# Kernel tuning notes

Measured on AMD Instinct MI355X. Metric: run time of the kernel, lower is better.

The kernel has to match this reference:

```python
import jax, jax.numpy as jnp
import numpy as np
import math

EPS = 1e-6
N_NODES = 25000
N_EDGES = 400000
F = 8            # multivector channels
NB = 8           # blades of Cl(3,0)
NORM_FACTOR = 1.0
SUBSPACES = np.array([1, 3, 3, 1])
REP = np.repeat(np.arange(4), SUBSPACES)   # grade index per blade: [0,1,1,1,2,2,2,3]
GRADES = np.array([0, 1, 1, 1, 2, 2, 2, 3])

def _build_cayley():
    # shortlex blade order for dim 3: 1, e1, e2, e3, e12, e13, e23, e123
    bitmaps = [0, 1, 2, 4, 3, 5, 6, 7]
    b2i = {b: i for i, b in enumerate(bitmaps)}
    def sign(a, b):
        a >>= 1
        s = 0
        while a:
            s += bin(a & b).count('1')
            a >>= 1
        return 1.0 if s % 2 == 0 else -1.0  # euclidean metric (1,1,1)
    C = np.zeros((NB, NB, NB), np.float32)
    for i, bi in enumerate(bitmaps):
        for j, bj in enumerate(bitmaps):
            C[i, b2i[bi ^ bj], j] = sign(bi, bj)   # cayley[left, out, right]
    return C

CAYLEY_NP = _build_cayley()

def _paths():
    p = np.zeros((4, 4, 4), bool)
    for a in range(4):
        for b in range(4):
            for c in range(4):
                blk = CAYLEY_NP[GRADES == a][:, GRADES == b][:, :, GRADES == c]
                p[a, b, c] = np.any(blk != 0)
    return np.nonzero(p)

PI, PJ, PK = _paths()
N_PATHS = len(PI)  # 20 for Cl(3,0)
CAYLEY = jnp.asarray(CAYLEY_NP)

def grade_qs(x):
    # per-grade quadratic form (euclidean: sum of squares), x: [..., 8] -> [..., 4]
    sq = x * x
    return jnp.concatenate([sq[..., 0:1],
                            sq[..., 1:4].sum(-1, keepdims=True),
                            sq[..., 4:7].sum(-1, keepdims=True),
                            sq[..., 7:8]], axis=-1)

def mv_linear(x, w, b=None):
    # w: [out, in, 4] grade-wise weights, repeat-interleaved over blades
    out = jnp.einsum('bmi,nmi->bni', x, w[:, :, REP])
    if b is not None:
        out = out.at[:, :, 0].add(b[0, :, 0])   # bias embedded in scalar blade
    return out

def mv_silu(x, a, b):
    q = grade_qs(x)
    inv = jnp.concatenate([x[..., :1], q[..., 1:]], axis=-1)  # scalar + mag2 per grade
    gate = jax.nn.sigmoid(a * inv + b)[..., REP]
    return gate * x

def sgp(x, w_right, w_geo, w_left, b_left, a_norm):
    # SteerableGeometricProductLayer with NormalizationLayer on the right input
    xr = mv_linear(x, w_right)
    norms = jnp.sqrt(grade_qs(xr))                       # [B,F,4]
    norms = jax.nn.sigmoid(a_norm) * (norms - 1.0) + 1.0
    xr = xr / (norms[..., REP] + EPS)
    W4 = jnp.zeros((F, 4, 4, 4), x.dtype).at[:, PI, PJ, PK].set(w_geo)
    W8 = W4[:, REP][:, :, REP][:, :, :, REP] * CAYLEY    # [F,8,8,8]
    geo = jnp.einsum('bni,nijk,bnk->bnj', x, W8, xr)
    return (mv_linear(x, w_left, b_left) + geo) / math.sqrt(2.0)

def mv_layernorm(x, a):
    n = jnp.sqrt((x * x).sum(-1, keepdims=True)).mean(axis=1, keepdims=True) + EPS
    return a[..., None] * x / n

def block(x, lin_w, lin_b, silu_a, silu_b, gp_wr, gp_w, gp_wl, gp_bl, gp_an, ln_a):
    # CEMLP block: MVLinear -> MVSiLU -> SteerableGeometricProduct -> MVLayerNorm
    x = mv_linear(x, lin_w, lin_b)
    x = mv_silu(x, silu_a, silu_b)
    x = sgp(x, gp_wr, gp_w, gp_wl, gp_bl, gp_an)
    return mv_layernorm(x, ln_a)

def setup_inputs() -> dict:
    key = jax.random.key(0)
    ks = jax.random.split(key, 12)
    h = jax.random.normal(ks[0], (N_NODES, F, NB), jnp.float32)
    edge_index = jax.random.randint(ks[1], (2, N_EDGES), 0, N_NODES)
    def linw(k, out_f, in_f):
        return jax.random.normal(k, (out_f, in_f, 4), jnp.float32) / math.sqrt(in_f)
    inp = dict(h=h, edge_index=edge_index)
    for pref, kk in (('e', 2), ('n', 7)):
        inp[pref + '_lin_w'] = linw(ks[kk], F, 2 * F)
        inp[pref + '_lin_b'] = jnp.zeros((1, F, 1), jnp.float32)
        inp[pref + '_silu_a'] = jnp.ones((1, F, 4), jnp.float32)
        inp[pref + '_silu_b'] = jnp.zeros((1, F, 4), jnp.float32)
        inp[pref + '_gp_wr'] = linw(ks[kk + 1], F, F)
        inp[pref + '_gp_w'] = jax.random.normal(ks[kk + 2], (F, N_PATHS), jnp.float32) / 2.0
        inp[pref + '_gp_wl'] = linw(ks[kk + 3], F, F)
        inp[pref + '_gp_bl'] = jnp.zeros((1, F, 1), jnp.float32)
        inp[pref + '_gp_an'] = jnp.zeros((F, 4), jnp.float32)
        inp[pref + '_ln_a'] = jnp.ones((1, F), jnp.float32)
    return inp

def reference(h, edge_index,
              e_lin_w, e_lin_b, e_silu_a, e_silu_b, e_gp_wr, e_gp_w, e_gp_wl, e_gp_bl, e_gp_an, e_ln_a,
              n_lin_w, n_lin_b, n_silu_a, n_silu_b, n_gp_wr, n_gp_w, n_gp_wl, n_gp_bl, n_gp_an, n_ln_a):
    row, col = edge_index[0], edge_index[1]
    # edge model: gather endpoint features, Clifford MLP block
    m = jnp.concatenate([h[row], h[col]], axis=1)          # [E, 2F, 8]
    m = block(m, e_lin_w, e_lin_b, e_silu_a, e_silu_b,
              e_gp_wr, e_gp_w, e_gp_wl, e_gp_bl, e_gp_an, e_ln_a)
    # unsorted_segment_sum on flattened multivectors, 'sum' aggregation
    agg = jax.ops.segment_sum(m.reshape(N_EDGES, -1), row, num_segments=N_NODES) / NORM_FACTOR
    agg = agg.reshape(N_NODES, F, NB)
    # node update: residual Clifford MLP block on [h, agg]
    upd = jnp.concatenate([h, agg], axis=1)                # [N, 2F, 8]
    upd = block(upd, n_lin_w, n_lin_b, n_silu_a, n_silu_b,
                n_gp_wr, n_gp_w, n_gp_wl, n_gp_bl, n_gp_an, n_ln_a)
    return h + upd
```

## Files before the change

kernel.cpp:

```cpp
#include <hip/hip_runtime.h>

#define NNODES 25000
#define NEDGES 400000
#define EPB 32
#define XSTR2 68
#define EPSF 1e-6f
#define RSQRT2 0.7071067811865476f

typedef _Float16 half8 __attribute__((ext_vector_type(8)));

static constexpr int GJ[64] = {
 0,1,2,3,4,5,6,7,
 1,0,4,5,2,3,7,6,
 2,4,0,6,1,7,3,5,
 3,5,6,0,7,1,2,4,
 4,2,1,7,0,6,5,3,
 5,3,7,1,6,0,4,2,
 6,7,3,2,5,4,0,1,
 7,6,5,4,3,2,1,0};
static constexpr int GS[64] = {
 1, 1, 1, 1, 1, 1, 1, 1,
 1, 1, 1, 1, 1, 1, 1, 1,
 1,-1, 1, 1,-1,-1, 1,-1,
 1,-1,-1, 1, 1,-1,-1, 1,
 1,-1, 1, 1,-1,-1, 1,-1,
 1,-1,-1, 1, 1,-1,-1, 1,
 1, 1,-1, 1,-1, 1,-1,-1,
 1, 1,-1, 1,-1, 1,-1,-1};
static constexpr int GP[64] = {
  0, 1, 1, 1, 2, 2, 2, 3,
  5, 4, 7, 7, 6, 6, 9, 8,
  5, 7, 4, 7, 6, 9, 6, 8,
  5, 7, 7, 4, 9, 6, 6, 8,
 13,11,11,15,10,14,14,12,
 13,11,15,11,14,10,14,12,
 13,15,11,11,14,14,10,12,
 19,18,18,18,17,17,17,16};

struct WP {
  const float *wlin, *blin, *asi, *bsi, *wr, *wg, *wl, *bl, *an, *aln;
};

__device__ __forceinline__ float sigm(float x) {
  return __builtin_amdgcn_rcpf(1.f + __expf(-x));
}
__device__ __forceinline__ float frcp(float x) { return __builtin_amdgcn_rcpf(x); }
__device__ __forceinline__ float fsqrt(float x) { return __builtin_amdgcn_sqrtf(x); }

__device__ __forceinline__ void wave_fence() {
  asm volatile("s_waitcnt lgkmcnt(0)" ::: "memory");
  __builtin_amdgcn_sched_barrier(0);
}

#define C_WR   0
#define C_WL   (C_WR + 288)
#define C_WG   (C_WL + 288)
#define C_BLIN (C_WG + 160)
#define C_ASI  (C_BLIN + 8)
#define C_BSI  (C_ASI + 32)
#define C_BL   (C_BSI + 32)
#define C_SA   (C_BL + 8)
#define C_SCC  (C_SA + 32)
#define C_ALN  (C_SCC + 32)
#define C_TOT  (C_ALN + 8)
#define C_WLIN C_TOT
#define CN_TOT (C_WLIN + 8*68)

__device__ __forceinline__ void stage_common(int tid, float* Ws, const WP& wp) {
  int t = tid;
  if (t < 256) Ws[C_WR + (t >> 5) * 36 + (t & 31)] = wp.wr[t];
  if (t < 256) Ws[C_WL + (t >> 5) * 36 + (t & 31)] = wp.wl[t];
  if (t < 160) Ws[C_WG + t] = wp.wg[t];
  if (t < 8)   Ws[C_BLIN + t] = wp.blin[t];
  if (t < 32)  Ws[C_ASI + t] = wp.asi[t];
  if (t < 32)  Ws[C_BSI + t] = wp.bsi[t];
  if (t < 8)   Ws[C_BL + t]  = wp.bl[t];
  if (t < 32)  {
    const float sv = sigm(wp.an[t]);
    Ws[C_SA + t]  = sv;
    Ws[C_SCC + t] = 1.f + EPSF - sv;
  }
  if (t < 8)   Ws[C_ALN + t] = wp.aln[t];
}

__device__ __forceinline__ void clifford_tail(float* __restrict__ X,
                                              const float* __restrict__ Ws,
                                              int n, const float* y, float* z)
{
  const float q1 = y[1]*y[1] + y[2]*y[2] + y[3]*y[3];
  const float q2 = y[4]*y[4] + y[5]*y[5] + y[6]*y[6];
  const float q3 = y[7]*y[7];
  const float g0 = sigm(Ws[C_ASI + n*4 + 0] * y[0] + Ws[C_BSI + n*4 + 0]);
  const float g1 = sigm(Ws[C_ASI + n*4 + 1] * q1  + Ws[C_BSI + n*4 + 1]);
  const float g2 = sigm(Ws[C_ASI + n*4 + 2] * q2  + Ws[C_BSI + n*4 + 2]);
  const float g3 = sigm(Ws[C_ASI + n*4 + 3] * q3  + Ws[C_BSI + n*4 + 3]);
  float s[8] = { g0*y[0], g1*y[1], g1*y[2], g1*y[3],
                 g2*y[4], g2*y[5], g2*y[6], g3*y[7] };
  *(float4*)&X[n*8]     = make_float4(s[0], s[1], s[2], s[3]);
  *(float4*)&X[n*8 + 4] = make_float4(s[4], s[5], s[6], s[7]);
  wave_fence();

  float xr[8], zl[8];
  #pragma unroll
  for (int i = 0; i < 8; ++i) { xr[i] = 0.f; zl[i] = 0.f; }
  #pragma unroll
  for (int m = 0; m < 8; ++m) {
    const float4 wr4 = *(const float4*)&Ws[C_WR + n * 36 + m * 4];
    const float4 wl4 = *(const float4*)&Ws[C_WL + n * 36 + m * 4];
    const float4 xa = *(const float4*)&X[m * 8];
    const float4 xb = *(const float4*)&X[m * 8 + 4];
    xr[0]=fmaf(xa.x,wr4.x,xr[0]); xr[1]=fmaf(xa.y,wr4.y,xr[1]); xr[2]=fmaf(xa.z,wr4.y,xr[2]); xr[3]=fmaf(xa.w,wr4.y,xr[3]);
    xr[4]=fmaf(xb.x,wr4.z,xr[4]); xr[5]=fmaf(xb.y,wr4.z,xr[5]); xr[6]=fmaf(xb.z,wr4.z,xr[6]); xr[7]=fmaf(xb.w,wr4.w,xr[7]);
    zl[0]=fmaf(xa.x,wl4.x,zl[0]); zl[1]=fmaf(xa.y,wl4.y,zl[1]); zl[2]=fmaf(xa.z,wl4.y,zl[2]); zl[3]=fmaf(xa.w,wl4.y,zl[3]);
    zl[4]=fmaf(xb.x,wl4.z,zl[4]); zl[5]=fmaf(xb.y,wl4.z,zl[5]); zl[6]=fmaf(xb.z,wl4.z,zl[6]); zl[7]=fmaf(xb.w,wl4.w,zl[7]);
  }
  zl[0] += Ws[C_BL + n];

  {
    const float t0 = fabsf(xr[0]);
    const float t1 = fsqrt(xr[1]*xr[1] + xr[2]*xr[2] + xr[3]*xr[3]);
    const float t2 = fsqrt(xr[4]*xr[4] + xr[5]*xr[5] + xr[6]*xr[6]);
    const float t3 = fabsf(xr[7]);
    const float d0 = frcp(fmaf(Ws[C_SA + n*4 + 0], t0, Ws[C_SCC + n*4 + 0]));
    const float d1 = frcp(fmaf(Ws[C_SA + n*4 + 1], t1, Ws[C_SCC + n*4 + 1]));
    const float d2 = frcp(fmaf(Ws[C_SA + n*4 + 2], t2, Ws[C_SCC + n*4 + 2]));
    const float d3 = frcp(fmaf(Ws[C_SA + n*4 + 3], t3, Ws[C_SCC + n*4 + 3]));
    xr[0] *= d0; xr[1] *= d1; xr[2] *= d1; xr[3] *= d1;
    xr[4] *= d2; xr[5] *= d2; xr[6] *= d2; xr[7] *= d3;
  }

  float geo[8];
  #pragma unroll
  for (int i = 0; i < 8; ++i) geo[i] = 0.f;
  {
    const int wgb = C_WG + n * 20;
    #pragma unroll
    for (int i = 0; i < 8; ++i) {
      #pragma unroll
      for (int k = 0; k < 8; ++k) {
        const float t = s[i] * xr[k];
        const float w = Ws[wgb + GP[i * 8 + k]];
        geo[GJ[i * 8 + k]] = fmaf(GS[i * 8 + k] > 0 ? w : -w, t, geo[GJ[i * 8 + k]]);
      }
    }
  }

  #pragma unroll
  for (int i = 0; i < 8; ++i) z[i] = (zl[i] + geo[i]) * RSQRT2;

  float sq = 0.f;
  #pragma unroll
  for (int i = 0; i < 8; ++i) sq = fmaf(z[i], z[i], sq);
  float nr = fsqrt(sq);
  nr += __shfl_xor(nr, 1);
  nr += __shfl_xor(nr, 2);
  nr += __shfl_xor(nr, 4);
  const float scale = Ws[C_ALN + n] * frcp(nr * 0.125f + EPSF);
  #pragma unroll
  for (int i = 0; i < 8; ++i) z[i] *= scale;
}

__global__ __launch_bounds__(1024)
void csr_scan_fast(const int* __restrict__ deg, int* __restrict__ ptr,
                   int* __restrict__ fill)
{
  __shared__ int wsum[16];
  const int t = threadIdx.x;
  const int base = t * 32;
  int d[32];
  int s = 0;
  #pragma unroll
  for (int i = 0; i < 8; ++i) {
    int idx = base + i * 4;
    int4 v = make_int4(0, 0, 0, 0);
    if (idx + 3 < NNODES) v = *(const int4*)(deg + idx);
    else {
      if (idx + 0 < NNODES) v.x = deg[idx + 0];
      if (idx + 1 < NNODES) v.y = deg[idx + 1];
      if (idx + 2 < NNODES) v.z = deg[idx + 2];
    }
    d[i*4+0] = v.x; d[i*4+1] = v.y; d[i*4+2] = v.z; d[i*4+3] = v.w;
    s += v.x + v.y + v.z + v.w;
  }
  const int lane = t & 63;
  int incl = s;
  #pragma unroll
  for (int off = 1; off < 64; off <<= 1) {
    int u = __shfl_up(incl, off);
    if (lane >= off) incl += u;
  }
  const int wv = t >> 6;
  if (lane == 63) wsum[wv] = incl;
  __syncthreads();
  if (t < 16) {
    int v = wsum[t];
    int inc = v;
    #pragma unroll
    for (int off = 1; off < 16; off <<= 1) {
      int u = __shfl_up(inc, off);
      if (t >= off) inc += u;
    }
    wsum[t] = inc - v;
  }
  __syncthreads();
  int run = wsum[wv] + (incl - s);
  #pragma unroll
  for (int i = 0; i < 8; ++i) {
    int idx = base + i * 4;
    int4 pv;
    pv.x = run; run += d[i*4+0];
    pv.y = run; run += d[i*4+1];
    pv.z = run; run += d[i*4+2];
    pv.w = run; run += d[i*4+3];
    if (idx + 3 < NNODES) {
      *(int4*)(ptr + idx)  = pv;
      *(int4*)(fill + idx) = pv;
    } else {
      if (idx + 0 < NNODES) { ptr[idx+0] = pv.x; fill[idx+0] = pv.x; }
      if (idx + 1 < NNODES) { ptr[idx+1] = pv.y; fill[idx+1] = pv.y; }
      if (idx + 2 < NNODES) { ptr[idx+2] = pv.z; fill[idx+2] = pv.z; }
    }
  }
  if (t == 1023) ptr[NNODES] = NEDGES;
}

#define PRE_BLOCKS ((NNODES + EPB - 1) / EPB)
#define CNT_BLOCKS ((NEDGES + 255) / 256)

__global__ __launch_bounds__(256)
void pre_count(const float* __restrict__ h,
               const float* __restrict__ wle,
               const float* __restrict__ ble,
               float* __restrict__ ue, float* __restrict__ ve,
               const int* __restrict__ eidx, int* __restrict__ deg)
{
  __shared__ __align__(16) float We[8 * 68];
  __shared__ __align__(16) float Xs[EPB * XSTR2];
  const int tid = threadIdx.x;

  if (blockIdx.x >= PRE_BLOCKS) {
    int e = (blockIdx.x - PRE_BLOCKS) * 256 + tid;
    if (e < NEDGES) atomicAdd(&deg[eidx[e]], 1);
    return;
  }

  for (int t = tid; t < 512; t += 256) We[(t >> 6) * 68 + (t & 63)] = wle[t];
  const int el = tid >> 3, n = tid & 7;
  const int item = blockIdx.x * EPB + el;
  float* X = &Xs[el * XSTR2];
  const bool act = item < NNODES;
  if (act) {
    const float4* ph = (const float4*)(h + (size_t)item * 64 + n * 8);
    *(float4*)&X[n * 8]     = ph[0];
    *(float4*)&X[n * 8 + 4] = ph[1];
  }
  __syncthreads();
  if (!act) return;
  float ua[8], va[8];
  #pragma unroll
  for (int i = 0; i < 8; ++i) { ua[i] = 0.f; va[i] = 0.f; }
  #pragma unroll
  for (int m = 0; m < 8; ++m) {
    const float4 xa = *(const float4*)&X[m * 8];
    const float4 xb = *(const float4*)&X[m * 8 + 4];
    const float4 wa = *(const float4*)&We[n * 68 + m * 4];
    const float4 wb = *(const float4*)&We[n * 68 + (m + 8) * 4];
    ua[0]=fmaf(xa.x,wa.x,ua[0]); ua[1]=fmaf(xa.y,wa.y,ua[1]); ua[2]=fmaf(xa.z,wa.y,ua[2]); ua[3]=fmaf(xa.w,wa.y,ua[3]);
    ua[4]=fmaf(xb.x,wa.z,ua[4]); ua[5]=fmaf(xb.y,wa.z,ua[5]); ua[6]=fmaf(xb.z,wa.z,ua[6]); ua[7]=fmaf(xb.w,wa.w,ua[7]);
    va[0]=fmaf(xa.x,wb.x,va[0]); va[1]=fmaf(xa.y,wb.y,va[1]); va[2]=fmaf(xa.z,wb.y,va[2]); va[3]=fmaf(xa.w,wb.y,va[3]);
    va[4]=fmaf(xb.x,wb.z,va[4]); va[5]=fmaf(xb.y,wb.z,va[5]); va[6]=fmaf(xb.z,wb.z,va[6]); va[7]=fmaf(xb.w,wb.w,va[7]);
  }
  ua[0] += ble[n];
  float4* pu = (float4*)(ue + (size_t)item * 64 + n * 8);
  pu[0] = make_float4(ua[0],ua[1],ua[2],ua[3]); pu[1] = make_float4(ua[4],ua[5],ua[6],ua[7]);
  float4* pv = (float4*)(ve + (size_t)item * 64 + n * 8);
  pv[0] = make_float4(va[0],va[1],va[2],va[3]); pv[1] = make_float4(va[4],va[5],va[6],va[7]);
}

__global__ __launch_bounds__(256) void csr_scatter(const int* __restrict__ eidx,
                                                   int* __restrict__ fill,
                                                   int* __restrict__ elist) {
  int e = blockIdx.x * 256 + threadIdx.x;
  if (e < NEDGES) {
    int pos = atomicAdd(&fill[eidx[e]], 1);
    elist[pos] = e;
  }
}

__global__ __launch_bounds__(256)
void cgenn7_edge(const int* __restrict__ eidx,
                 const int* __restrict__ elist,
                 const float* __restrict__ ue, const float* __restrict__ ve,
                 _Float16* __restrict__ msgh, WP wp)
{
  __shared__ __align__(16) float Ws[C_TOT];
  __shared__ __align__(16) float Xs[EPB * XSTR2];
  const int tid = threadIdx.x;
  const int el = tid >> 3, n = tid & 7;
  const int p = blockIdx.x * EPB + el;

  const int e = elist[p];
  const int r = eidx[e];
  const int c = eidx[NEDGES + e];
  const float4* pu = (const float4*)(ue + (size_t)r * 64 + n * 8);
  const float4 u0 = pu[0], u1 = pu[1];
  const float4* pv = (const float4*)(ve + (size_t)c * 64 + n * 8);
  const float4 v0 = pv[0], v1 = pv[1];

  stage_common(tid, Ws, wp);
  __syncthreads();

  float y[8] = { u0.x+v0.x, u0.y+v0.y, u0.z+v0.z, u0.w+v0.w,
                 u1.x+v1.x, u1.y+v1.y, u1.z+v1.z, u1.w+v1.w };

  float z[8];
  clifford_tail(&Xs[el * XSTR2], Ws, n, y, z);

  half8 hm;
  hm[0]=(_Float16)z[0]; hm[1]=(_Float16)z[1]; hm[2]=(_Float16)z[2]; hm[3]=(_Float16)z[3];
  hm[4]=(_Float16)z[4]; hm[5]=(_Float16)z[5]; hm[6]=(_Float16)z[6]; hm[7]=(_Float16)z[7];
  *(half8*)(msgh + (size_t)p * 64 + n * 8) = hm;
}

#define NPB 4
__global__ __launch_bounds__(256)
void cgenn7_node(const float* __restrict__ h,
                 const _Float16* __restrict__ msgh,
                 const int* __restrict__ ptr,
                 float* __restrict__ out, WP wp)
{
  __shared__ __align__(16) float Ws[CN_TOT];
  __shared__ __align__(16) float Xs[NPB * 132];
  const int tid  = threadIdx.x;
  const int wv   = tid >> 6;
  const int slot = (tid >> 3) & 7;
  const int n    = tid & 7;
  const int nid  = blockIdx.x * NPB + wv;
  float* X = &Xs[wv * 132];

  stage_common(tid, Ws, wp);
  for (int t = tid; t < 512; t += 256)
    Ws[C_WLIN + (t >> 6) * 68 + (t & 63)] = wp.wlin[t];

  const int beg = ptr[nid], end = ptr[nid + 1];

  float a[8];
  #pragma unroll
  for (int i = 0; i < 8; ++i) a[i] = 0.f;
  const _Float16* mb = msgh + (size_t)n * 8;
  for (int p = beg + slot; p < end; p += 8) {
    const half8 m = *(const half8*)(mb + (size_t)p * 64);
    #pragma unroll
    for (int i = 0; i < 8; ++i) a[i] += (float)m[i];
  }
  #pragma unroll
  for (int i = 0; i < 8; ++i) {
    a[i] += __shfl_xor(a[i], 8);
    a[i] += __shfl_xor(a[i], 16);
    a[i] += __shfl_xor(a[i], 32);
  }

  __syncthreads();

  if (slot == 0) {
    float hr[8];
    const float4* ph = (const float4*)(h + (size_t)nid * 64 + n * 8);
    const float4 h0 = ph[0], h1 = ph[1];
    hr[0]=h0.x; hr[1]=h0.y; hr[2]=h0.z; hr[3]=h0.w;
    hr[4]=h1.x; hr[5]=h1.y; hr[6]=h1.z; hr[7]=h1.w;
    *(float4*)&X[n*8]         = h0;
    *(float4*)&X[n*8 + 4]     = h1;
    *(float4*)&X[(8+n)*8]     = make_float4(a[0], a[1], a[2], a[3]);
    *(float4*)&X[(8+n)*8 + 4] = make_float4(a[4], a[5], a[6], a[7]);
    wave_fence();

    float y[8];
    #pragma unroll
    for (int i = 0; i < 8; ++i) y[i] = 0.f;
    #pragma unroll
    for (int m = 0; m < 16; ++m) {
      const float4 w4 = *(const float4*)&Ws[C_WLIN + n * 68 + m * 4];
      const float4 xa = *(const float4*)&X[m * 8];
      const float4 xb = *(const float4*)&X[m * 8 + 4];
      y[0]=fmaf(xa.x,w4.x,y[0]); y[1]=fmaf(xa.y,w4.y,y[1]); y[2]=fmaf(xa.z,w4.y,y[2]); y[3]=fmaf(xa.w,w4.y,y[3]);
      y[4]=fmaf(xb.x,w4.z,y[4]); y[5]=fmaf(xb.y,w4.z,y[5]); y[6]=fmaf(xb.z,w4.z,y[6]); y[7]=fmaf(xb.w,w4.w,y[7]);
    }
    y[0] += Ws[C_BLIN + n];

    float z[8];
    clifford_tail(X, Ws, n, y, z);

    float4* po = (float4*)(out + (size_t)nid * 64 + n * 8);
    po[0] = make_float4(hr[0]+z[0], hr[1]+z[1], hr[2]+z[2], hr[3]+z[3]);
    po[1] = make_float4(hr[4]+z[4], hr[5]+z[5], hr[6]+z[6], hr[7]+z[7]);
  }
}

template<bool IS_NODE>
__global__ __launch_bounds__(256)
void cgenn_block(const float* __restrict__ h,
                 const int* __restrict__ eidx,
                 float* agg_out, WP wp)
{
  __shared__ __align__(16) float Ws[CN_TOT];
  __shared__ __align__(16) float Xs[EPB * 132];
  const int tid = threadIdx.x;
  stage_common(tid, Ws, wp);
  for (int t = tid; t < 512; t += 256)
    Ws[C_WLIN + (t >> 6) * 68 + (t & 63)] = wp.wlin[t];
  const int el = tid >> 3;
  const int n  = tid & 7;
  const int item = blockIdx.x * EPB + el;
  float* X = &Xs[el * 132];
  bool active = true;
  int r = 0;
  float hr[8];
  if (IS_NODE) {
    active = (item < NNODES);
    if (active) {
      const float4* ph = (const float4*)(h + (size_t)item * 64 + n * 8);
      float4 a0 = ph[0], a1 = ph[1];
      hr[0]=a0.x; hr[1]=a0.y; hr[2]=a0.z; hr[3]=a0.w;
      hr[4]=a1.x; hr[5]=a1.y; hr[6]=a1.z; hr[7]=a1.w;
      *(float4*)&X[n*8]     = a0;
      *(float4*)&X[n*8 + 4] = a1;
      const float4* pa = (const float4*)(agg_out + (size_t)item * 64 + n * 8);
      *(float4*)&X[(8+n)*8]     = pa[0];
      *(float4*)&X[(8+n)*8 + 4] = pa[1];
    }
  } else {
    r = eidx[item];
    const int c = eidx[NEDGES + item];
    const float4* ph = (const float4*)(h + (size_t)r * 64 + n * 8);
    float4 a0 = ph[0], a1 = ph[1];
    const float4* pc = (const float4*)(h + (size_t)c * 64 + n * 8);
    float4 b0 = pc[0], b1 = pc[1];
    *(float4*)&X[n*8]       = a0;  *(float4*)&X[n*8 + 4]     = a1;
    *(float4*)&X[(8+n)*8]   = b0;  *(float4*)&X[(8+n)*8 + 4] = b1;
  }
  __syncthreads();
  float y[8];
  #pragma unroll
  for (int i = 0; i < 8; ++i) y[i] = 0.f;
  #pragma unroll
  for (int m = 0; m < 16; ++m) {
    const float4 w4 = *(const float4*)&Ws[C_WLIN + n * 68 + m * 4];
    const float4 xa = *(const float4*)&X[m * 8];
    const float4 xb = *(const float4*)&X[m * 8 + 4];
    y[0]=fmaf(xa.x,w4.x,y[0]); y[1]=fmaf(xa.y,w4.y,y[1]); y[2]=fmaf(xa.z,w4.y,y[2]); y[3]=fmaf(xa.w,w4.y,y[3]);
    y[4]=fmaf(xb.x,w4.z,y[4]); y[5]=fmaf(xb.y,w4.z,y[5]); y[6]=fmaf(xb.z,w4.z,y[6]); y[7]=fmaf(xb.w,w4.w,y[7]);
  }
  y[0] += Ws[C_BLIN + n];
  float z[8];
  clifford_tail(X, Ws, n, y, z);
  if (IS_NODE) {
    if (active) {
      float4* po = (float4*)(agg_out + (size_t)item * 64 + n * 8);
      po[0] = make_float4(hr[0]+z[0], hr[1]+z[1], hr[2]+z[2], hr[3]+z[3]);
      po[1] = make_float4(hr[4]+z[4], hr[5]+z[5], hr[6]+z[6], hr[7]+z[7]);
    }
  } else {
    float* dst = agg_out + (size_t)r * 64 + n * 8;
    #pragma unroll
    for (int i = 0; i < 8; ++i) atomicAdd(dst + i, z[i]);
  }
}

extern "C" void kernel_launch(void* const* d_in, const int* in_sizes, int n_in,
                              void* d_out, int out_size, void* d_ws, size_t ws_size,
                              hipStream_t stream)
{
  (void)in_sizes; (void)n_in; (void)out_size;
  const float* h   = (const float*)d_in[0];
  const int* eidx  = (const int*)d_in[1];
  WP we = { (const float*)d_in[2],  (const float*)d_in[3],  (const float*)d_in[4],
            (const float*)d_in[5],  (const float*)d_in[6],  (const float*)d_in[7],
            (const float*)d_in[8],  (const float*)d_in[9],  (const float*)d_in[10],
            (const float*)d_in[11] };
  WP wn = { (const float*)d_in[12], (const float*)d_in[13], (const float*)d_in[14],
            (const float*)d_in[15], (const float*)d_in[16], (const float*)d_in[17],
            (const float*)d_in[18], (const float*)d_in[19], (const float*)d_in[20],
            (const float*)d_in[21] };
  float* out = (float*)d_out;

  const size_t mhsz   = (size_t)NEDGES * 64 * sizeof(_Float16);
  const size_t nodef  = (size_t)NNODES * 64 * sizeof(float);
  const size_t elsz   = (size_t)NEDGES * sizeof(int);
  const size_t degsz  = (size_t)25008 * sizeof(int);
  const size_t fillsz = (size_t)25008 * sizeof(int);
  const size_t need   = mhsz + 2 * nodef + elsz + degsz + fillsz;

  if (ws_size >= need) {
    char* base = (char*)d_ws;
    _Float16* msgh = (_Float16*)base;   base += mhsz;
    float* ue   = (float*)base;         base += nodef;
    float* ve   = (float*)base;         base += nodef;
    int* elist  = (int*)base;           base += elsz;
    int* deg    = (int*)base;           base += degsz;
    int* fill   = (int*)base;

    hipMemsetAsync(deg, 0, (NNODES + 1) * sizeof(int), stream);
    pre_count<<<dim3(PRE_BLOCKS + CNT_BLOCKS), dim3(256), 0, stream>>>(
        h, we.wlin, we.blin, ue, ve, eidx, deg);
    csr_scan_fast<<<dim3(1), dim3(1024), 0, stream>>>(deg, deg, fill);
    csr_scatter<<<dim3(CNT_BLOCKS), dim3(256), 0, stream>>>(eidx, fill, elist);
    cgenn7_edge<<<dim3(NEDGES / EPB), dim3(256), 0, stream>>>(
        eidx, elist, ue, ve, msgh, we);
    cgenn7_node<<<dim3(NNODES / NPB), dim3(256), 0, stream>>>(h, msgh, deg, out, wn);
  } else {
    hipMemsetAsync(d_out, 0, (size_t)NNODES * 64 * sizeof(float), stream);
    cgenn_block<false><<<dim3(NEDGES / EPB), dim3(256), 0, stream>>>(h, eidx, out, we);
    cgenn_block<true><<<dim3((NNODES + EPB - 1) / EPB), dim3(256), 0, stream>>>(h, eidx, out, wn);
  }
}
```

Measured before the change: 154.1 us.

## Record per-edge atomic rank during counting and drop the CSR scatter kernel

The degree-count atomics now also store each edge's rank within its source node. The edge kernel then walks edges in their original order and computes the message slot as ptr[row]+rank. This removes the separate scatter kernel, its second round of atomics, the fill array and the elist indirection. In exchange the edge kernel reads in edge order rather than row-sorted order, so gathers of ue are less local, and its fp16 message writes become scattered.

```diff
diff --git a/kernel.cpp b/kernel.cpp
--- a/kernel.cpp
+++ b/kernel.cpp
@@ -161,8 +161,7 @@
 }
 
 __global__ __launch_bounds__(1024)
-void csr_scan_fast(const int* __restrict__ deg, int* __restrict__ ptr,
-                   int* __restrict__ fill)
+void csr_scan_fast(const int* __restrict__ deg, int* __restrict__ ptr)
 {
   __shared__ int wsum[16];
   const int t = threadIdx.x;
@@ -213,12 +212,11 @@
     pv.z = run; run += d[i*4+2];
     pv.w = run; run += d[i*4+3];
     if (idx + 3 < NNODES) {
-      *(int4*)(ptr + idx)  = pv;
-      *(int4*)(fill + idx) = pv;
+      *(int4*)(ptr + idx) = pv;
     } else {
-      if (idx + 0 < NNODES) { ptr[idx+0] = pv.x; fill[idx+0] = pv.x; }
-      if (idx + 1 < NNODES) { ptr[idx+1] = pv.y; fill[idx+1] = pv.y; }
-      if (idx + 2 < NNODES) { ptr[idx+2] = pv.z; fill[idx+2] = pv.z; }
+      if (idx + 0 < NNODES) ptr[idx+0] = pv.x;
+      if (idx + 1 < NNODES) ptr[idx+1] = pv.y;
+      if (idx + 2 < NNODES) ptr[idx+2] = pv.z;
     }
   }
   if (t == 1023) ptr[NNODES] = NEDGES;
@@ -232,7 +230,8 @@
                const float* __restrict__ wle,
                const float* __restrict__ ble,
                float* __restrict__ ue, float* __restrict__ ve,
-               const int* __restrict__ eidx, int* __restrict__ deg)
+               const int* __restrict__ eidx, int* __restrict__ deg,
+               int* __restrict__ rank)
 {
   __shared__ __align__(16) float We[8 * 68];
   __shared__ __align__(16) float Xs[EPB * XSTR2];
@@ -240,7 +239,7 @@
 
   if (blockIdx.x >= PRE_BLOCKS) {
     int e = (blockIdx.x - PRE_BLOCKS) * 256 + tid;
-    if (e < NEDGES) atomicAdd(&deg[eidx[e]], 1);
+    if (e < NEDGES) rank[e] = atomicAdd(&deg[eidx[e]], 1);
     return;
   }
 
@@ -277,19 +276,10 @@
   pv[0] = make_float4(va[0],va[1],va[2],va[3]); pv[1] = make_float4(va[4],va[5],va[6],va[7]);
 }
 
-__global__ __launch_bounds__(256) void csr_scatter(const int* __restrict__ eidx,
-                                                   int* __restrict__ fill,
-                                                   int* __restrict__ elist) {
-  int e = blockIdx.x * 256 + threadIdx.x;
-  if (e < NEDGES) {
-    int pos = atomicAdd(&fill[eidx[e]], 1);
-    elist[pos] = e;
-  }
-}
-
 __global__ __launch_bounds__(256)
-void cgenn7_edge(const int* __restrict__ eidx,
-                 const int* __restrict__ elist,
+void cgenn8_edge(const int* __restrict__ eidx,
+                 const int* __restrict__ rank,
+                 const int* __restrict__ ptr,
                  const float* __restrict__ ue, const float* __restrict__ ve,
                  _Float16* __restrict__ msgh, WP wp)
 {
@@ -297,11 +287,11 @@
   __shared__ __align__(16) float Xs[EPB * XSTR2];
   const int tid = threadIdx.x;
   const int el = tid >> 3, n = tid & 7;
-  const int p = blockIdx.x * EPB + el;
-
-  const int e = elist[p];
+  const int e = blockIdx.x * EPB + el;
+
   const int r = eidx[e];
   const int c = eidx[NEDGES + e];
+  const int p = ptr[r] + rank[e];
   const float4* pu = (const float4*)(ue + (size_t)r * 64 + n * 8);
   const float4 u0 = pu[0], u1 = pu[1];
   const float4* pv = (const float4*)(ve + (size_t)c * 64 + n * 8);
@@ -485,28 +475,27 @@
 
   const size_t mhsz   = (size_t)NEDGES * 64 * sizeof(_Float16);
   const size_t nodef  = (size_t)NNODES * 64 * sizeof(float);
-  const size_t elsz   = (size_t)NEDGES * sizeof(int);
+  const size_t rksz   = (size_t)NEDGES * sizeof(int);
   const size_t degsz  = (size_t)25008 * sizeof(int);
-  const size_t fillsz = (size_t)25008 * sizeof(int);
-  const size_t need   = mhsz + 2 * nodef + elsz + degsz + fillsz;
+  const size_t ptrsz  = (size_t)25008 * sizeof(int);
+  const size_t need   = mhsz + 2 * nodef + rksz + degsz + ptrsz;
 
   if (ws_size >= need) {
     char* base = (char*)d_ws;
     _Float16* msgh = (_Float16*)base;   base += mhsz;
     float* ue   = (float*)base;         base += nodef;
     float* ve   = (float*)base;         base += nodef;
-    int* elist  = (int*)base;           base += elsz;
+    int* rank   = (int*)base;           base += rksz;
     int* deg    = (int*)base;           base += degsz;
-    int* fill   = (int*)base;
+    int* ptr    = (int*)base;
 
     hipMemsetAsync(deg, 0, (NNODES + 1) * sizeof(int), stream);
     pre_count<<<dim3(PRE_BLOCKS + CNT_BLOCKS), dim3(256), 0, stream>>>(
-        h, we.wlin, we.blin, ue, ve, eidx, deg);
-    csr_scan_fast<<<dim3(1), dim3(1024), 0, stream>>>(deg, deg, fill);
-    csr_scatter<<<dim3(CNT_BLOCKS), dim3(256), 0, stream>>>(eidx, fill, elist);
-    cgenn7_edge<<<dim3(NEDGES / EPB), dim3(256), 0, stream>>>(
-        eidx, elist, ue, ve, msgh, we);
-    cgenn7_node<<<dim3(NNODES / NPB), dim3(256), 0, stream>>>(h, msgh, deg, out, wn);
+        h, we.wlin, we.blin, ue, ve, eidx, deg, rank);
+    csr_scan_fast<<<dim3(1), dim3(1024), 0, stream>>>(deg, ptr);
+    cgenn8_edge<<<dim3(NEDGES / EPB), dim3(256), 0, stream>>>(
+        eidx, rank, ptr, ue, ve, msgh, we);
+    cgenn7_node<<<dim3(NNODES / NPB), dim3(256), 0, stream>>>(h, msgh, ptr, out, wn);
   } else {
     hipMemsetAsync(d_out, 0, (size_t)NNODES * 64 * sizeof(float), stream);
     cgenn_block<false><<<dim3(NEDGES / EPB), dim3(256), 0, stream>>>(h, eidx, out, we);
```

Measured after the change: 128.4 us. 1.2x faster.
